# Performance work log

Hardware: AMD Instinct MI355X
Metric: run time of the kernel (lower is better)

The kernel has to match this reference:

```python
import jax, jax.numpy as jnp
import numpy as np

TOTAL_OUTPUTS = 50000
PER_CLASS = 224
N_CLASSES = int(np.ceil(TOTAL_OUTPUTS / PER_CLASS))  # 224
B, T, D = 4, 512, 1024


def setup_inputs() -> dict:
    key = jax.random.key(0)
    k1, k2, k3, k4 = jax.random.split(key, 4)
    scale_top = float(np.sqrt(2.0 / (D + N_CLASSES)))      # glorot-ish
    scale_bot = float(np.sqrt(2.0 / (D + PER_CLASS)))
    return {
        "x": jax.random.normal(k1, (B, T, D), dtype=jnp.float32),
        "target": jax.random.randint(k2, (B, T), 0, TOTAL_OUTPUTS, dtype=jnp.int32),
        "top_weights": jax.random.normal(k3, (D, N_CLASSES), dtype=jnp.float32) * scale_top,
        "top_bias": jnp.zeros((N_CLASSES,), dtype=jnp.float32),
        "bottom_weights": jax.random.normal(k4, (N_CLASSES, D, PER_CLASS), dtype=jnp.float32) * scale_bot,
        "bottom_bias": jnp.zeros((N_CLASSES, PER_CLASS), dtype=jnp.float32),
    }


def reference(x, target, top_weights, top_bias, bottom_weights, bottom_bias):
    # Flatten (batch, time) -> samples, as in call()
    b, t, d = x.shape
    xf = x.reshape(b * t, d)                      # (N, D)
    tf = target.reshape(-1)                       # (N,)

    # Top-level dense softmax over classes
    p_top = jax.nn.softmax(xf @ top_weights + top_bias, axis=-1)  # (N, n_classes)

    # Decompose target into (class, within-class) indices, as in theano h_softmax
    cls = tf // PER_CLASS                         # (N,)
    within = tf % PER_CLASS                       # (N,)

    # Gather per-sample bottom expert weights and compute small GEMM + softmax
    w_c = bottom_weights[cls]                     # (N, D, per_class)  <- irregular gather
    b_c = bottom_bias[cls]                        # (N, per_class)
    bot_logits = jnp.einsum('nd,ndp->np', xf, w_c) + b_c
    p_bot = jax.nn.softmax(bot_logits, axis=-1)   # (N, per_class)

    n_idx = jnp.arange(xf.shape[0])
    px = p_top[n_idx, cls] * p_bot[n_idx, within]  # (N,) target probabilities
    return px.reshape(b, t, -1)                    # (B, T, 1)
```

## Files before the change

kernel.cpp:

```cpp
#include <hip/hip_runtime.h>

#define NSAMP 2048
#define DIM 1024
#define NCLS 224
#define PERCLS 224
#define CH 16
#define KSL 256
#define NSLICE 4
#define BOTBLKS (NCLS * NSLICE)
#define TOPBLKS ((NSAMP / CH) * NSLICE)
#define NTILE 32
#define TILE_B 7168
#define SLOT_F 2048

struct Ws {
  int cls[NSAMP];
  int within[NSAMP];
  int order[NSAMP];
  int offsets[NCLS + 1];
  int pad_[3];
  float top_part[NSLICE][NSAMP][NCLS];
  float bot_part[NSLICE][NSAMP][PERCLS];
};

__global__ __launch_bounds__(256) void prep_kernel(const int* __restrict__ target,
                                                   Ws* __restrict__ ws) {
  __shared__ int cnt[NCLS];
  __shared__ int cur[NCLS];
  __shared__ int sc[256];
  int tid = threadIdx.x;
  for (int c = tid; c < NCLS; c += 256) cnt[c] = 0;
  __syncthreads();
  for (int n = tid; n < NSAMP; n += 256) {
    int t = target[n];
    int c = t / PERCLS;
    ws->cls[n] = c;
    ws->within[n] = t - c * PERCLS;
    atomicAdd(&cnt[c], 1);
  }
  __syncthreads();
  int v = (tid < NCLS) ? cnt[tid] : 0;
  sc[tid] = v;
  __syncthreads();
  for (int off = 1; off < 256; off <<= 1) {
    int a = (tid >= off) ? sc[tid - off] : 0;
    __syncthreads();
    sc[tid] += a;
    __syncthreads();
  }
  if (tid < NCLS) {
    int excl = sc[tid] - cnt[tid];
    ws->offsets[tid] = excl;
    cur[tid] = excl;
  }
  if (tid == 0) ws->offsets[NCLS] = NSAMP;
  __syncthreads();
  for (int n = tid; n < NSAMP; n += 256) {
    int c = ws->cls[n];
    int pos = atomicAdd(&cur[c], 1);
    ws->order[pos] = n;
  }
}

__global__ __launch_bounds__(128) void partial_kernel(const float* __restrict__ x,
                                                      const float* __restrict__ tw,
                                                      const float* __restrict__ bw,
                                                      Ws* __restrict__ ws) {
  __shared__ float xs[CH][KSL];
  __shared__ float wl[3 * SLOT_F];
  const int tid = threadIdx.x;
  const int lane = tid & 63;
  const int wv = tid >> 6;
  const int bid = blockIdx.x;

  const bool is_bot = bid < BOTBLKS;
  int n0 = 0, c = 0, bs, start = 0, K = CH;
  if (is_bot) {
    bs = bid & 3;
    c = bid >> 2;
    start = ws->offsets[c];
    K = ws->offsets[c + 1] - start;
    if (K == 0) return;
  } else {
    int b = bid - BOTBLKS;
    bs = b & 3;
    n0 = (b >> 2) * CH;
  }
  const float* Wslice = is_bot
      ? (bw + (size_t)c * (DIM * PERCLS) + (size_t)(bs * KSL) * PERCLS)
      : (tw + (size_t)(bs * KSL) * NCLS);

  typedef const __attribute__((address_space(1))) unsigned int gu32;
  typedef __attribute__((address_space(3))) unsigned int lu32;

  auto stage_tile = [&](int t) {
    const char* base = (const char*)Wslice + (size_t)t * TILE_B;
    float* slot = &wl[(t % 3) * SLOT_F];
#pragma unroll
    for (int j = 0; j < 4; ++j) {
      int u = wv * 4 + j;
      int off = u * 1024 + lane * 16;
      int soff = (off < TILE_B) ? off : (off - 1024);
      __builtin_amdgcn_global_load_lds((gu32*)(base + soff),
                                       (lu32*)(slot + u * 256), 16, 0, 0);
    }
  };

  float4 acc[8];

  auto compute_tile = [&](int t) {
    if (lane < 56) {
      const float* slot = &wl[(t % 3) * SLOT_F];
#pragma unroll
      for (int g = 0; g < 2; ++g) {
        float4 w0 = *(const float4*)&slot[(g * 4 + 0) * 224 + lane * 4];
        float4 w1 = *(const float4*)&slot[(g * 4 + 1) * 224 + lane * 4];
        float4 w2 = *(const float4*)&slot[(g * 4 + 2) * 224 + lane * 4];
        float4 w3 = *(const float4*)&slot[(g * 4 + 3) * 224 + lane * 4];
#pragma unroll
        for (int s = 0; s < 8; ++s) {
          float4 xv = *(const float4*)&xs[wv * 8 + s][t * 8 + g * 4];
          acc[s].x = fmaf(xv.x, w0.x, acc[s].x);
          acc[s].y = fmaf(xv.x, w0.y, acc[s].y);
          acc[s].z = fmaf(xv.x, w0.z, acc[s].z);
          acc[s].w = fmaf(xv.x, w0.w, acc[s].w);
          acc[s].x = fmaf(xv.y, w1.x, acc[s].x);
          acc[s].y = fmaf(xv.y, w1.y, acc[s].y);
          acc[s].z = fmaf(xv.y, w1.z, acc[s].z);
          acc[s].w = fmaf(xv.y, w1.w, acc[s].w);
          acc[s].x = fmaf(xv.z, w2.x, acc[s].x);
          acc[s].y = fmaf(xv.z, w2.y, acc[s].y);
          acc[s].z = fmaf(xv.z, w2.z, acc[s].z);
          acc[s].w = fmaf(xv.z, w2.w, acc[s].w);
          acc[s].x = fmaf(xv.w, w3.x, acc[s].x);
          acc[s].y = fmaf(xv.w, w3.y, acc[s].y);
          acc[s].z = fmaf(xv.w, w3.z, acc[s].z);
          acc[s].w = fmaf(xv.w, w3.w, acc[s].w);
        }
      }
    }
  };

  for (int chunk = 0; chunk < K; chunk += CH) {
    const int S = min(CH, K - chunk);
    __syncthreads();

#pragma unroll
    for (int pass = 0; pass < 8; ++pass) {
      int i = tid + pass * 128;
      int ss = i >> 6;
      int q = i & 63;
      int n;
      if (is_bot) n = ws->order[start + min(chunk + ss, K - 1)];
      else        n = n0 + ss;
      ((float4*)xs)[i] = *(const float4*)(x + (size_t)n * DIM + bs * KSL + q * 4);
    }
    __syncthreads();

#pragma unroll
    for (int s = 0; s < 8; ++s) acc[s] = make_float4(0.f, 0.f, 0.f, 0.f);

    stage_tile(0);
    stage_tile(1);

    for (int t = 0; t < NTILE - 2; ++t) {
      asm volatile("s_waitcnt vmcnt(4)" ::: "memory");
      __builtin_amdgcn_sched_barrier(0);
      __builtin_amdgcn_s_barrier();
      __builtin_amdgcn_sched_barrier(0);
      stage_tile(t + 2);
      compute_tile(t);
    }
    asm volatile("s_waitcnt vmcnt(4)" ::: "memory");
    __builtin_amdgcn_sched_barrier(0);
    __builtin_amdgcn_s_barrier();
    __builtin_amdgcn_sched_barrier(0);
    compute_tile(NTILE - 2);
    asm volatile("s_waitcnt vmcnt(0)" ::: "memory");
    __builtin_amdgcn_sched_barrier(0);
    __builtin_amdgcn_s_barrier();
    __builtin_amdgcn_sched_barrier(0);
    compute_tile(NTILE - 1);

    if (lane < 56) {
      if (is_bot) {
#pragma unroll
        for (int s = 0; s < 8; ++s) {
          int sl = wv * 8 + s;
          if (sl < S) {
            int n = ws->order[start + chunk + sl];
            *(float4*)&ws->bot_part[bs][n][lane * 4] = acc[s];
          }
        }
      } else {
#pragma unroll
        for (int s = 0; s < 8; ++s)
          *(float4*)&ws->top_part[bs][n0 + wv * 8 + s][lane * 4] = acc[s];
      }
    }
  }
}

__global__ __launch_bounds__(256) void final_kernel(const float* __restrict__ tb,
                                                    const float* __restrict__ bb,
                                                    const Ws* __restrict__ ws,
                                                    float* __restrict__ out) {
  __shared__ float lt[8][NCLS];
  __shared__ float lb[8][NCLS];
  const int tid = threadIdx.x;
  const int n0 = blockIdx.x * 8;
  const int p = tid;

  if (p < NCLS) {
    float tbias = tb[p];
#pragma unroll
    for (int s = 0; s < 8; ++s) {
      int n = n0 + s;
      int c = ws->cls[n];
      float t = tbias;
      float b = bb[(size_t)c * PERCLS + p];
#pragma unroll
      for (int dc = 0; dc < NSLICE; ++dc) t += ws->top_part[dc][n][p];
#pragma unroll
      for (int dc = 0; dc < NSLICE; ++dc) b += ws->bot_part[dc][n][p];
      lt[s][p] = t;
      lb[s][p] = b;
    }
  }
  __syncthreads();

  const int wv = tid >> 6, lane = tid & 63;
  for (int s = wv * 2; s < wv * 2 + 2; ++s) {
    const int n = n0 + s;
    float v[4], mx = -INFINITY;
#pragma unroll
    for (int j = 0; j < 4; ++j) {
      int pp = lane + 64 * j;
      v[j] = (pp < NCLS) ? lt[s][pp] : -INFINITY;
      mx = fmaxf(mx, v[j]);
    }
#pragma unroll
    for (int m = 32; m >= 1; m >>= 1) mx = fmaxf(mx, __shfl_xor(mx, m));
    float sum = 0.f;
#pragma unroll
    for (int j = 0; j < 4; ++j) {
      int pp = lane + 64 * j;
      if (pp < NCLS) sum += expf(v[j] - mx);
    }
#pragma unroll
    for (int m = 32; m >= 1; m >>= 1) sum += __shfl_xor(sum, m);
    float pt = expf(lt[s][ws->cls[n]] - mx) / sum;

    float mb = -INFINITY;
#pragma unroll
    for (int j = 0; j < 4; ++j) {
      int pp = lane + 64 * j;
      v[j] = (pp < NCLS) ? lb[s][pp] : -INFINITY;
      mb = fmaxf(mb, v[j]);
    }
#pragma unroll
    for (int m = 32; m >= 1; m >>= 1) mb = fmaxf(mb, __shfl_xor(mb, m));
    float sb = 0.f;
#pragma unroll
    for (int j = 0; j < 4; ++j) {
      int pp = lane + 64 * j;
      if (pp < NCLS) sb += expf(v[j] - mb);
    }
#pragma unroll
    for (int m = 32; m >= 1; m >>= 1) sb += __shfl_xor(sb, m);
    float pb = expf(lb[s][ws->within[n]] - mb) / sb;

    if (lane == 0) out[n] = pt * pb;
  }
}

extern "C" void kernel_launch(void* const* d_in, const int* in_sizes, int n_in,
                              void* d_out, int out_size, void* d_ws, size_t ws_size,
                              hipStream_t stream) {
  const float* x  = (const float*)d_in[0];
  const int* tgt  = (const int*)d_in[1];
  const float* tw = (const float*)d_in[2];
  const float* tb = (const float*)d_in[3];
  const float* bw = (const float*)d_in[4];
  const float* bb = (const float*)d_in[5];
  float* out = (float*)d_out;
  Ws* ws = (Ws*)d_ws;

  prep_kernel<<<1, 256, 0, stream>>>(tgt, ws);
  partial_kernel<<<BOTBLKS + TOPBLKS, 128, 0, stream>>>(x, tw, bw, ws);
  final_kernel<<<NSAMP / 8, 256, 0, stream>>>(tb, bb, ws, out);
}
```

Measured before the change: 86.05 us.

## Split K across waves with private double-buffered weight tiles and LDS reduction

Each of the two waves now owns half of the K slice and streams its own weight tiles into a private double buffer, so the per-tile block-wide barriers are gone. Each wave computes all 16 samples with 16 float4 accumulators. A cross-wave reduction through LDS runs at the end. This removes the s_barrier per tile and reuses each loaded weight row across 16 samples instead of 8, at the cost of doubled accumulator registers and an extra reduction step.

```diff
diff --git a/kernel.cpp b/kernel.cpp
--- a/kernel.cpp
+++ b/kernel.cpp
@@ -9,9 +9,9 @@
 #define NSLICE 4
 #define BOTBLKS (NCLS * NSLICE)
 #define TOPBLKS ((NSAMP / CH) * NSLICE)
-#define NTILE 32
+#define WTILES 16
 #define TILE_B 7168
-#define SLOT_F 2048
+#define SLOT_F 1792
 
 struct Ws {
   int cls[NSAMP];
@@ -67,10 +67,10 @@
                                                       const float* __restrict__ bw,
                                                       Ws* __restrict__ ws) {
   __shared__ float xs[CH][KSL];
-  __shared__ float wl[3 * SLOT_F];
+  __shared__ float wl[2][2][SLOT_F];
   const int tid = threadIdx.x;
   const int lane = tid & 63;
-  const int wv = tid >> 6;
+  const int kg = tid >> 6;
   const int bid = blockIdx.x;
 
   const bool is_bot = bid < BOTBLKS;
@@ -89,28 +89,26 @@
   const float* Wslice = is_bot
       ? (bw + (size_t)c * (DIM * PERCLS) + (size_t)(bs * KSL) * PERCLS)
       : (tw + (size_t)(bs * KSL) * NCLS);
+  const float* Wwave = Wslice + (size_t)kg * (WTILES * SLOT_F);
 
   typedef const __attribute__((address_space(1))) unsigned int gu32;
   typedef __attribute__((address_space(3))) unsigned int lu32;
 
   auto stage_tile = [&](int t) {
-    const char* base = (const char*)Wslice + (size_t)t * TILE_B;
-    float* slot = &wl[(t % 3) * SLOT_F];
-#pragma unroll
-    for (int j = 0; j < 4; ++j) {
-      int u = wv * 4 + j;
-      int off = u * 1024 + lane * 16;
-      int soff = (off < TILE_B) ? off : (off - 1024);
-      __builtin_amdgcn_global_load_lds((gu32*)(base + soff),
-                                       (lu32*)(slot + u * 256), 16, 0, 0);
+    const char* base = (const char*)Wwave + (size_t)t * TILE_B;
+    char* slot = (char*)&wl[kg][t & 1][0];
+#pragma unroll
+    for (int u = 0; u < 7; ++u) {
+      __builtin_amdgcn_global_load_lds((gu32*)(base + u * 1024 + lane * 16),
+                                       (lu32*)(slot + u * 1024), 16, 0, 0);
     }
   };
 
-  float4 acc[8];
+  float4 acc[16];
 
   auto compute_tile = [&](int t) {
     if (lane < 56) {
-      const float* slot = &wl[(t % 3) * SLOT_F];
+      const float* slot = &wl[kg][t & 1][0];
 #pragma unroll
       for (int g = 0; g < 2; ++g) {
         float4 w0 = *(const float4*)&slot[(g * 4 + 0) * 224 + lane * 4];
@@ -118,8 +116,8 @@
         float4 w2 = *(const float4*)&slot[(g * 4 + 2) * 224 + lane * 4];
         float4 w3 = *(const float4*)&slot[(g * 4 + 3) * 224 + lane * 4];
 #pragma unroll
-        for (int s = 0; s < 8; ++s) {
-          float4 xv = *(const float4*)&xs[wv * 8 + s][t * 8 + g * 4];
+        for (int s = 0; s < 16; ++s) {
+          float4 xv = *(const float4*)&xs[s][kg * 128 + t * 8 + g * 4];
           acc[s].x = fmaf(xv.x, w0.x, acc[s].x);
           acc[s].y = fmaf(xv.x, w0.y, acc[s].y);
           acc[s].z = fmaf(xv.x, w0.z, acc[s].z);
@@ -155,47 +153,56 @@
       else        n = n0 + ss;
       ((float4*)xs)[i] = *(const float4*)(x + (size_t)n * DIM + bs * KSL + q * 4);
     }
-    __syncthreads();
-
-#pragma unroll
-    for (int s = 0; s < 8; ++s) acc[s] = make_float4(0.f, 0.f, 0.f, 0.f);
 
     stage_tile(0);
     stage_tile(1);
-
-    for (int t = 0; t < NTILE - 2; ++t) {
-      asm volatile("s_waitcnt vmcnt(4)" ::: "memory");
+    asm volatile("s_waitcnt lgkmcnt(0)" ::: "memory");
+    __builtin_amdgcn_sched_barrier(0);
+    __builtin_amdgcn_s_barrier();
+    __builtin_amdgcn_sched_barrier(0);
+
+#pragma unroll
+    for (int s = 0; s < 16; ++s) acc[s] = make_float4(0.f, 0.f, 0.f, 0.f);
+
+    for (int t = 0; t < WTILES - 2; ++t) {
+      asm volatile("s_waitcnt vmcnt(7)" ::: "memory");
       __builtin_amdgcn_sched_barrier(0);
-      __builtin_amdgcn_s_barrier();
+      compute_tile(t);
       __builtin_amdgcn_sched_barrier(0);
       stage_tile(t + 2);
-      compute_tile(t);
-    }
-    asm volatile("s_waitcnt vmcnt(4)" ::: "memory");
-    __builtin_amdgcn_sched_barrier(0);
-    __builtin_amdgcn_s_barrier();
-    __builtin_amdgcn_sched_barrier(0);
-    compute_tile(NTILE - 2);
+    }
+    asm volatile("s_waitcnt vmcnt(7)" ::: "memory");
+    __builtin_amdgcn_sched_barrier(0);
+    compute_tile(WTILES - 2);
     asm volatile("s_waitcnt vmcnt(0)" ::: "memory");
     __builtin_amdgcn_sched_barrier(0);
-    __builtin_amdgcn_s_barrier();
-    __builtin_amdgcn_sched_barrier(0);
-    compute_tile(NTILE - 1);
-
-    if (lane < 56) {
+    compute_tile(WTILES - 1);
+
+    __syncthreads();
+    float4* mb = (float4*)xs;
+    if (kg == 1 && lane < 56) {
+#pragma unroll
+      for (int s = 0; s < 16; ++s) mb[s * 56 + lane] = acc[s];
+    }
+    __syncthreads();
+    if (kg == 0 && lane < 56) {
       if (is_bot) {
 #pragma unroll
-        for (int s = 0; s < 8; ++s) {
-          int sl = wv * 8 + s;
-          if (sl < S) {
-            int n = ws->order[start + chunk + sl];
+        for (int s = 0; s < 16; ++s) {
+          if (s < S) {
+            float4 o = mb[s * 56 + lane];
+            acc[s].x += o.x; acc[s].y += o.y; acc[s].z += o.z; acc[s].w += o.w;
+            int n = ws->order[start + chunk + s];
             *(float4*)&ws->bot_part[bs][n][lane * 4] = acc[s];
           }
         }
       } else {
 #pragma unroll
-        for (int s = 0; s < 8; ++s)
-          *(float4*)&ws->top_part[bs][n0 + wv * 8 + s][lane * 4] = acc[s];
+        for (int s = 0; s < 16; ++s) {
+          float4 o = mb[s * 56 + lane];
+          acc[s].x += o.x; acc[s].y += o.y; acc[s].z += o.z; acc[s].w += o.w;
+          *(float4*)&ws->top_part[bs][n0 + s][lane * 4] = acc[s];
+        }
       }
     }
   }
```

New measurement: 88.91 us. 3.3% more time.
